# Performance work log

Measured on AMD Instinct MI355X. Metric: run time of the kernel, lower is better.

Reference implementation:

```python
import jax, jax.numpy as jnp
import numpy as np

N_NODES = 100000


def _gcn_edges(edge_index, num_nodes):
    # Add self-loops and compute symmetric GCN normalization per edge.
    src = jnp.concatenate([edge_index[0], jnp.arange(num_nodes, dtype=edge_index.dtype)])
    dst = jnp.concatenate([edge_index[1], jnp.arange(num_nodes, dtype=edge_index.dtype)])
    deg = jnp.zeros((num_nodes,), jnp.float32).at[dst].add(1.0)
    dinv = jnp.where(deg > 0, jax.lax.rsqrt(deg), 0.0)
    norm = dinv[src] * dinv[dst]  # [E+N]
    return src, dst, norm


def _gcn_conv(x, W, b, src, dst, norm, num_nodes):
    h = x @ W                         # [N, d_out] transform first (d_out <= d_in)
    msg = h[src] * norm[:, None]      # [E, d_out] gather + scale
    agg = jax.ops.segment_sum(msg, dst, num_segments=num_nodes)
    return agg + b


def setup_inputs() -> dict:
    key = jax.random.key(0)
    k = jax.random.split(key, 8)
    n, e, d_in, d_out = N_NODES, 1600000, 128, 64
    hid = 2 * d_out
    s = lambda fan: 1.0 / np.sqrt(fan)
    return {
        "x": jax.random.normal(k[0], (n, d_in), jnp.float32),
        "edge_index": jax.random.randint(k[1], (2, e), 0, n, jnp.int64),
        "W1": jax.random.normal(k[2], (d_in, hid), jnp.float32) * s(d_in),
        "b1": jnp.zeros((hid,), jnp.float32),
        "Wmu": jax.random.normal(k[3], (hid, d_out), jnp.float32) * s(hid),
        "bmu": jnp.zeros((d_out,), jnp.float32),
        "Wls": jax.random.normal(k[4], (hid, d_out), jnp.float32) * s(hid),
        "bls": jnp.zeros((d_out,), jnp.float32),
    }


def reference(x, edge_index, W1, b1, Wmu, bmu, Wls, bls):
    n = x.shape[0]
    src, dst, norm = _gcn_edges(edge_index, n)
    h = jax.nn.relu(_gcn_conv(x, W1, b1, src, dst, norm, n))
    mu = _gcn_conv(h, Wmu, bmu, src, dst, norm, n)
    logstd = _gcn_conv(h, Wls, bls, src, dst, norm, n)
    return mu, logstd
```

## Files before the change

kernel.cpp:

```cpp
#include <hip/hip_runtime.h>

#define DIN 128
#define HID 128
#define DOUT 64
#define NCHUNK 784
#define BSH 9
#define NB1MAX 256
#define BSLACK 1540

typedef unsigned short ushort_t;
typedef unsigned int uint_t;
typedef __attribute__((ext_vector_type(4))) short s4v;
typedef __attribute__((ext_vector_type(4))) float f4v;

#if defined(__has_builtin)
#if __has_builtin(__builtin_amdgcn_mfma_f32_16x16x16bf16_1k)
#define MFMA16(a, b, c) __builtin_amdgcn_mfma_f32_16x16x16bf16_1k(a, b, c, 0, 0, 0)
#endif
#endif
#ifndef MFMA16
static __device__ inline f4v mfma16_asm(s4v a, s4v b, f4v c) {
  asm volatile("v_mfma_f32_16x16x16_bf16 %0, %1, %2, %0" : "+v"(c) : "v"(a), "v"(b));
  return c;
}
#define MFMA16(a, b, c) mfma16_asm(a, b, c)
#endif

static inline int ceil_div(int a, int b) { return (a + b - 1) / b; }

__device__ inline ushort_t f2bf(float f) {
  uint_t u = __float_as_uint(f);
  u += 0x7fff + ((u >> 16) & 1);
  return (ushort_t)(u >> 16);
}
__device__ inline uint_t pack2bf(float a, float b) {
  return (uint_t)f2bf(a) | ((uint_t)f2bf(b) << 16);
}
__device__ inline float2 bf2x2(uint_t u) {
  return make_float2(__uint_as_float(u << 16), __uint_as_float(u & 0xffff0000u));
}

__device__ inline int blk_scan_incl(int v, int* ws, int nw) {
  int t = threadIdx.x, lane = t & 63, w = t >> 6;
#pragma unroll
  for (int d = 1; d < 64; d <<= 1) {
    int u = __shfl_up(v, d, 64);
    if (lane >= d) v += u;
  }
  if (lane == 63) ws[w] = v;
  __syncthreads();
  if (w == 0) {
    int s = (lane < nw) ? ws[lane] : 0;
    for (int d = 1; d < nw; d <<= 1) {
      int u = __shfl_up(s, d, 64);
      if (lane >= d) s += u;
    }
    if (lane < nw) ws[lane] = s;
  }
  __syncthreads();
  if (w > 0) v += ws[w - 1];
  return v;
}


__global__ __launch_bounds__(512) void k_setup(const int* __restrict__ dst, int E, int CH,
                                               int nb1, int* __restrict__ counts,
                                               const float* __restrict__ x,
                                               const float* __restrict__ W1,
                                               const float* __restrict__ Wmu,
                                               const float* __restrict__ Wls,
                                               ushort_t* __restrict__ Wt2,
                                               ushort_t* __restrict__ xWb,
                                               ushort_t* __restrict__ h,
                                               float* __restrict__ dinv, int N, int G1) {
  __shared__ ushort_t Ws[128][132];
  __shared__ uint_t cnt[NB1MAX];
  int b = blockIdx.x, t = threadIdx.x;
  if (b < G1) {
#pragma unroll
    for (int it = 0; it < 16; it++) {
      int k = it * 8 + ((t >> 7) << 1);
      int j = t & 127;
      float a = W1[k * 128 + j];
      float bb = W1[(k + 1) * 128 + j];
      *(uint_t*)&Ws[j][k] = pack2bf(a, bb);
    }
    __syncthreads();
    int w = t >> 6, lane = t & 63;
    int rl = lane & 15, g = lane >> 4;
    int row = b * 128 + w * 16 + rl;
    bool valid = row < N;
    const float* Ar = x + (size_t)row * DIN + 4 * g;
    s4v af[8];
#pragma unroll
    for (int kk = 0; kk < 8; kk++) {
      float4 v = make_float4(0.f, 0.f, 0.f, 0.f);
      if (valid) v = *(const float4*)(Ar + kk * 16);
      s4v a;
      a[0] = (short)f2bf(v.x);
      a[1] = (short)f2bf(v.y);
      a[2] = (short)f2bf(v.z);
      a[3] = (short)f2bf(v.w);
      af[kk] = a;
    }
    f4v acc[8];
#pragma unroll
    for (int ct = 0; ct < 8; ct++) acc[ct] = (f4v)0.f;
#pragma unroll
    for (int kk = 0; kk < 8; kk++) {
      int ko = kk * 16 + 4 * g;
#pragma unroll
      for (int ct = 0; ct < 8; ct++) {
        s4v bb = *(s4v*)&Ws[ct * 16 + rl][ko];
        acc[ct] = MFMA16(af[kk], bb, acc[ct]);
      }
    }
    int gr0 = b * 128 + w * 16 + 4 * g;
#pragma unroll
    for (int i = 0; i < 4; i++) {
      int gr = gr0 + i;
      if (gr < N) {
#pragma unroll
        for (int ct = 0; ct < 8; ct++)
          xWb[(size_t)gr * HID + ct * 16 + rl] = f2bf(acc[ct][i]);
      }
    }
  } else if (b < G1 + NCHUNK) {
    int c = b - G1;
    for (int i = t; i < nb1; i += 512) cnt[i] = 0;
    __syncthreads();
    int e0 = c * CH, e1 = min(E, e0 + CH);
    for (int i = e0 + t; i < e1; i += 512) atomicAdd(&cnt[((uint_t)dst[i]) >> BSH], 1u);
    __syncthreads();
    for (int i = t; i < nb1; i += 512) counts[c * nb1 + i] = (int)cnt[i];
  } else if (b < G1 + NCHUNK + 32) {
    int idx = (b - G1 - NCHUNK) * 512 + t;
    int j = idx >> 7, k = idx & 127;
    Wt2[j * 128 + k] = f2bf(j < 64 ? Wmu[k * 64 + j] : Wls[k * 64 + (j - 64)]);
  } else {
    if (t < 64) ((uint_t*)(xWb + (size_t)N * HID))[t] = 0;
    else if (t < 128) ((uint_t*)(h + (size_t)N * HID))[t - 64] = 0;
    else if (t == 128) dinv[N] = 0.f;
  }
}

__global__ __launch_bounds__(256) void k_bscan(const int* __restrict__ counts, int nb1,
                                               int* __restrict__ chunk_off,
                                               int* __restrict__ btot) {
  __shared__ int ws[8];
  __shared__ int shc;
  int b = blockIdx.x, t = threadIdx.x;
  int carry = 0;
#pragma unroll
  for (int r = 0; r < NCHUNK / 256 + 1; r++) {
    int idx = r * 256 + t;
    int v = (idx < NCHUNK) ? counts[idx * nb1 + b] : 0;
    int incl = blk_scan_incl(v, ws, 4) + carry;
    if (idx < NCHUNK) chunk_off[idx * nb1 + b] = incl - v;
    if (t == 255) shc = incl;
    __syncthreads();
    carry = shc;
  }
  if (t == 0) btot[b] = carry;
}

__global__ __launch_bounds__(256) void k_bscatter(const int* __restrict__ src,
                                                  const int* __restrict__ dst, int E, int CH,
                                                  int nb1, const int* __restrict__ btot,
                                                  const int* __restrict__ chunk_off,
                                                  uint_t* __restrict__ tmp) {
  __shared__ int ws[8];
  __shared__ uint_t cur[NB1MAX];
  int t = threadIdx.x, c = blockIdx.x;
  {
    int v = (t < nb1) ? btot[t] : 0;
    int incl = blk_scan_incl(v, ws, 4);
    if (t < nb1) cur[t] = (uint_t)(incl - v + chunk_off[c * nb1 + t]);
  }
  __syncthreads();
  int e0 = c * CH, e1 = min(E, e0 + CH);
  for (int i = e0 + t; i < e1; i += 256) {
    uint_t d = (uint_t)dst[i];
    uint_t s = (uint_t)src[i];
    uint_t p = atomicAdd(&cur[d >> BSH], 1u);
    tmp[p] = ((d & ((1u << BSH) - 1)) << 17) | s;
  }
}

__global__ __launch_bounds__(512) void k_bfinal(const uint_t* __restrict__ tmp,
                                                const int* __restrict__ btot, int N, int nb1,
                                                uint_t* __restrict__ csr,
                                                int* __restrict__ row_ptr,
                                                int* __restrict__ row_end,
                                                float* __restrict__ dinv) {
  __shared__ int ws[8];
  __shared__ int sseg0, sseg1;
  __shared__ uint_t cnt[1 << BSH];
  __shared__ uint_t ppfx[1 << BSH];
  __shared__ uint_t cur[1 << BSH];
  int b = blockIdx.x, t = threadIdx.x;
  {
    int v = (t < nb1) ? btot[t] : 0;
    int incl = blk_scan_incl(v, ws, 8);
    if (t == b) {
      sseg0 = incl - v;
      sseg1 = incl;
    }
  }
  for (int i = t; i < (1 << BSH); i += 512) cnt[i] = 0;
  __syncthreads();
  int seg0 = sseg0, seg1 = sseg1;
  int pb = ((seg0 + 3) & ~3) + BSLACK * b;
  for (int i = seg0 + t; i < seg1; i += 512) atomicAdd(&cnt[tmp[i] >> 17], 1u);
  __syncthreads();
  if (t < 64) {
    uint_t pc[8];
    uint_t s = 0;
#pragma unroll
    for (int k = 0; k < 8; k++) {
      pc[k] = (cnt[t * 8 + k] + 3u) & ~3u;
      s += pc[k];
    }
    int incl = (int)s;
#pragma unroll
    for (int d = 1; d < 64; d <<= 1) {
      int u = __shfl_up(incl, d, 64);
      if (t >= d) incl += u;
    }
    uint_t excl = (uint_t)incl - s;
#pragma unroll
    for (int k = 0; k < 8; k++) {
      ppfx[t * 8 + k] = excl;
      excl += pc[k];
    }
  }
  __syncthreads();
  int nd0 = b << BSH;
  for (int i = t; i < (1 << BSH); i += 512) {
    cur[i] = ppfx[i];
    int g = nd0 + i;
    if (g < N) {
      row_ptr[g] = pb + (int)ppfx[i];
      row_end[g] = pb + (int)(ppfx[i] + ((cnt[i] + 3u) & ~3u));
      dinv[g] = rsqrtf((float)cnt[i] + 1.0f);
    }
  }
  __syncthreads();
  for (int i = seg0 + t; i < seg1; i += 512) {
    uint_t v = tmp[i];
    uint_t pos = atomicAdd(&cur[v >> 17], 1u);
    csr[pb + (int)pos] = v & 0x1FFFFu;
  }
  __syncthreads();
  for (int i = t; i < (1 << BSH); i += 512) {
    uint_t e0 = cur[i];
    uint_t e1 = ppfx[i] + ((cnt[i] + 3u) & ~3u);
    for (uint_t k = e0; k < e1; k++) csr[pb + (int)k] = (uint_t)N;
  }
}


__global__ __launch_bounds__(256) void k_agg(const ushort_t* __restrict__ H,
                                             const int* __restrict__ row_ptr,
                                             const int* __restrict__ row_end,
                                             const uint_t* __restrict__ csr,
                                             const float* __restrict__ dinv,
                                             const float* __restrict__ bias,
                                             ushort_t* __restrict__ out, int n) {
  int node = (blockIdx.x * blockDim.x + threadIdx.x) >> 6;
  int lane = threadIdx.x & 63;
  if (node >= n) return;
  const char* Hb = (const char*)H;
  const char* Db = (const char*)dinv;
  uint_t loff = (uint_t)lane << 2;
  float dn = dinv[node];
  int j = row_ptr[node], end = row_end[node];
  float2 hs = bf2x2(*(const uint_t*)(Hb + ((size_t)(((uint_t)node << 8) | loff))));
  float ax = dn * hs.x, ay = dn * hs.y;
  if (j < end) {
    uint4 c = *(const uint4*)(csr + j);
    while (true) {
      int jn = j + 4;
      bool more = jn < end;
      uint4 cn;
      if (more) cn = *(const uint4*)(csr + jn);
      float w0 = *(const float*)(Db + (size_t)(c.x << 2));
      float w1 = *(const float*)(Db + (size_t)(c.y << 2));
      float w2 = *(const float*)(Db + (size_t)(c.z << 2));
      float w3 = *(const float*)(Db + (size_t)(c.w << 2));
      uint_t v0 = *(const uint_t*)(Hb + (size_t)((c.x << 8) | loff));
      uint_t v1 = *(const uint_t*)(Hb + (size_t)((c.y << 8) | loff));
      uint_t v2 = *(const uint_t*)(Hb + (size_t)((c.z << 8) | loff));
      uint_t v3 = *(const uint_t*)(Hb + (size_t)((c.w << 8) | loff));
      float2 f0 = bf2x2(v0), f1 = bf2x2(v1), f2 = bf2x2(v2), f3 = bf2x2(v3);
      ax += w0 * f0.x; ay += w0 * f0.y;
      ax += w1 * f1.x; ay += w1 * f1.y;
      ax += w2 * f2.x; ay += w2 * f2.y;
      ax += w3 * f3.x; ay += w3 * f3.y;
      if (!more) break;
      c = cn;
      j = jn;
    }
  }
  ax = fmaxf(dn * ax + bias[2 * lane], 0.f) * dn;
  ay = fmaxf(dn * ay + bias[2 * lane + 1], 0.f) * dn;
  ((uint_t*)out)[(size_t)node * 64 + lane] = pack2bf(ax, ay);
}


__global__ __launch_bounds__(1024) void k_agg2g(const ushort_t* __restrict__ H,
                                                const int* __restrict__ row_ptr,
                                                const int* __restrict__ row_end,
                                                const uint_t* __restrict__ csr,
                                                const float* __restrict__ dinv,
                                                const ushort_t* __restrict__ Wt2,
                                                const float* __restrict__ bmu,
                                                const float* __restrict__ bls,
                                                float* __restrict__ out, int n) {
  __shared__ ushort_t rows[16][132];
  int t = threadIdx.x, w = t >> 6, lane = t & 63;
  int node = blockIdx.x * 16 + w;
  float ax = 0.f, ay = 0.f;
  if (node < n) {
    const char* Hb = (const char*)H;
    uint_t loff = (uint_t)lane << 2;
    float dn = dinv[node];
    int j = row_ptr[node], end = row_end[node];
    float2 hs = bf2x2(*(const uint_t*)(Hb + ((size_t)(((uint_t)node << 8) | loff))));
    ax = hs.x;
    ay = hs.y;
    if (j < end) {
      uint4 c = *(const uint4*)(csr + j);
      while (true) {
        int jn = j + 4;
        bool more = jn < end;
        uint4 cn;
        if (more) cn = *(const uint4*)(csr + jn);
        uint_t v0 = *(const uint_t*)(Hb + (size_t)((c.x << 8) | loff));
        uint_t v1 = *(const uint_t*)(Hb + (size_t)((c.y << 8) | loff));
        uint_t v2 = *(const uint_t*)(Hb + (size_t)((c.z << 8) | loff));
        uint_t v3 = *(const uint_t*)(Hb + (size_t)((c.w << 8) | loff));
        float2 f0 = bf2x2(v0), f1 = bf2x2(v1), f2 = bf2x2(v2), f3 = bf2x2(v3);
        ax += f0.x + f1.x;
        ay += f0.y + f1.y;
        ax += f2.x + f3.x;
        ay += f2.y + f3.y;
        if (!more) break;
        c = cn;
        j = jn;
      }
    }
    ax *= dn;
    ay *= dn;
  }
  *(uint_t*)&rows[w][2 * lane] = pack2bf(ax, ay);
  __syncthreads();
  if (w < 8) {
    int ct = w, rl = lane & 15, g = lane >> 4;
    f4v acc = (f4v)0.f;
#pragma unroll
    for (int kk = 0; kk < 8; kk++) {
      s4v a = *(s4v*)&rows[rl][kk * 16 + 4 * g];
      s4v b = *(const s4v*)(Wt2 + (size_t)(ct * 16 + rl) * 128 + kk * 16 + 4 * g);
      acc = MFMA16(a, b, acc);
    }
    int col = ct * 16 + rl;
    float bv = (col < 64) ? bmu[col] : bls[col - 64];
    size_t obase = (col < 64) ? 0 : (size_t)n * DOUT;
    int cc = col & 63;
#pragma unroll
    for (int i = 0; i < 4; i++) {
      int nd = blockIdx.x * 16 + 4 * g + i;
      if (nd < n) out[obase + (size_t)nd * DOUT + cc] = acc[i] + bv;
    }
  }
}


extern "C" void kernel_launch(void* const* d_in, const int* in_sizes, int n_in,
                              void* d_out, int out_size, void* d_ws, size_t ws_size,
                              hipStream_t stream) {
  const float* x   = (const float*)d_in[0];
  const int*   ei  = (const int*)d_in[1];
  const float* W1  = (const float*)d_in[2];
  const float* b1  = (const float*)d_in[3];
  const float* Wmu = (const float*)d_in[4];
  const float* bmu = (const float*)d_in[5];
  const float* Wls = (const float*)d_in[6];
  const float* bls = (const float*)d_in[7];
  float* out = (float*)d_out;

  const int N = in_sizes[0] / DIN;
  const int E = in_sizes[1] / 2;
  const int* esrc = ei;
  const int* edst = ei + E;
  const int nb1 = ceil_div(N, 1 << BSH);
  const int CH = ceil_div(E, NCHUNK);
  const int G1 = ceil_div(N, 128);

  char* ws = (char*)d_ws;
  size_t off = 0;
  auto alloc = [&](size_t bytes) -> void* {
    void* p = ws + off;
    off = (off + bytes + 255) & ~(size_t)255;
    return p;
  };
  ushort_t* xWb   = (ushort_t*)alloc((size_t)(N + 1) * HID * sizeof(ushort_t));
  ushort_t* h     = (ushort_t*)alloc((size_t)(N + 1) * HID * sizeof(ushort_t));
  uint_t* csr     = (uint_t*)alloc(((size_t)E + (size_t)(BSLACK + 8) * nb1 + 16) * 4);
  uint_t* tmp     = (uint_t*)alloc((size_t)E * 4);
  int* counts     = (int*)alloc((size_t)NCHUNK * nb1 * 4);
  int* chunk_off  = (int*)alloc((size_t)NCHUNK * nb1 * 4);
  int* btot       = (int*)alloc((size_t)nb1 * 4);
  int* row_ptr    = (int*)alloc((size_t)N * 4);
  int* row_end    = (int*)alloc((size_t)N * 4);
  float* dinv     = (float*)alloc((size_t)(N + 1) * 4);
  ushort_t* wt2b  = (ushort_t*)alloc((size_t)HID * HID * 2);
  (void)ws_size; (void)n_in; (void)out_size;

  k_setup<<<G1 + NCHUNK + 33, 512, 0, stream>>>(edst, E, CH, nb1, counts, x, W1, Wmu, Wls,
                                                wt2b, xWb, h, dinv, N, G1);
  k_bscan<<<nb1, 256, 0, stream>>>(counts, nb1, chunk_off, btot);
  k_bscatter<<<NCHUNK, 256, 0, stream>>>(esrc, edst, E, CH, nb1, btot, chunk_off, tmp);
  k_bfinal<<<nb1, 512, 0, stream>>>(tmp, btot, N, nb1, csr, row_ptr, row_end, dinv);

  k_agg<<<ceil_div(N, 4), 256, 0, stream>>>(xWb, row_ptr, row_end, csr, dinv, b1, h, N);

  k_agg2g<<<ceil_div(N, 16), 1024, 0, stream>>>(h, row_ptr, row_end, csr, dinv, wt2b, bmu, bls,
                                                out, N);
}
```

Baseline: 249.4 us.

## Split fused layer-2 aggregate+GEMM into separate aggregation and MFMA GEMM kernels

The fused layer-2 kernel, which aggregated 16 nodes per 1024-thread block and then ran a small MFMA GEMM on 8 of its 16 waves, is split in two. One 256-thread kernel does the neighbour aggregation and writes bf16 rows into the xWb buffer. A separate GEMM kernel stages the weight matrix in LDS and computes 64 rows by 128 columns per block with MFMA. The aim is to remove the block-wide barrier and the idle waves during the GEMM, which limited latency hiding in the gather. The cost is an extra kernel launch and a round trip through global memory for the intermediate.

```diff
diff --git a/kernel.cpp b/kernel.cpp
--- a/kernel.cpp
+++ b/kernel.cpp
@@ -260,13 +260,13 @@
 }
 
 
-__global__ __launch_bounds__(256) void k_agg(const ushort_t* __restrict__ H,
-                                             const int* __restrict__ row_ptr,
-                                             const int* __restrict__ row_end,
-                                             const uint_t* __restrict__ csr,
-                                             const float* __restrict__ dinv,
-                                             const float* __restrict__ bias,
-                                             ushort_t* __restrict__ out, int n) {
+__global__ __launch_bounds__(256) void k_agg1(const ushort_t* __restrict__ H,
+                                              const int* __restrict__ row_ptr,
+                                              const int* __restrict__ row_end,
+                                              const uint_t* __restrict__ csr,
+                                              const float* __restrict__ dinv,
+                                              const float* __restrict__ bias,
+                                              ushort_t* __restrict__ out, int n) {
   int node = (blockIdx.x * blockDim.x + threadIdx.x) >> 6;
   int lane = threadIdx.x & 63;
   if (node >= n) return;
@@ -308,70 +308,106 @@
 }
 
 
-__global__ __launch_bounds__(1024) void k_agg2g(const ushort_t* __restrict__ H,
-                                                const int* __restrict__ row_ptr,
-                                                const int* __restrict__ row_end,
-                                                const uint_t* __restrict__ csr,
-                                                const float* __restrict__ dinv,
-                                                const ushort_t* __restrict__ Wt2,
-                                                const float* __restrict__ bmu,
-                                                const float* __restrict__ bls,
-                                                float* __restrict__ out, int n) {
-  __shared__ ushort_t rows[16][132];
-  int t = threadIdx.x, w = t >> 6, lane = t & 63;
-  int node = blockIdx.x * 16 + w;
-  float ax = 0.f, ay = 0.f;
-  if (node < n) {
-    const char* Hb = (const char*)H;
-    uint_t loff = (uint_t)lane << 2;
-    float dn = dinv[node];
-    int j = row_ptr[node], end = row_end[node];
-    float2 hs = bf2x2(*(const uint_t*)(Hb + ((size_t)(((uint_t)node << 8) | loff))));
-    ax = hs.x;
-    ay = hs.y;
-    if (j < end) {
-      uint4 c = *(const uint4*)(csr + j);
-      while (true) {
-        int jn = j + 4;
-        bool more = jn < end;
-        uint4 cn;
-        if (more) cn = *(const uint4*)(csr + jn);
-        uint_t v0 = *(const uint_t*)(Hb + (size_t)((c.x << 8) | loff));
-        uint_t v1 = *(const uint_t*)(Hb + (size_t)((c.y << 8) | loff));
-        uint_t v2 = *(const uint_t*)(Hb + (size_t)((c.z << 8) | loff));
-        uint_t v3 = *(const uint_t*)(Hb + (size_t)((c.w << 8) | loff));
-        float2 f0 = bf2x2(v0), f1 = bf2x2(v1), f2 = bf2x2(v2), f3 = bf2x2(v3);
-        ax += f0.x + f1.x;
-        ay += f0.y + f1.y;
-        ax += f2.x + f3.x;
-        ay += f2.y + f3.y;
-        if (!more) break;
-        c = cn;
-        j = jn;
-      }
-    }
-    ax *= dn;
-    ay *= dn;
-  }
-  *(uint_t*)&rows[w][2 * lane] = pack2bf(ax, ay);
-  __syncthreads();
-  if (w < 8) {
-    int ct = w, rl = lane & 15, g = lane >> 4;
-    f4v acc = (f4v)0.f;
-#pragma unroll
-    for (int kk = 0; kk < 8; kk++) {
-      s4v a = *(s4v*)&rows[rl][kk * 16 + 4 * g];
-      s4v b = *(const s4v*)(Wt2 + (size_t)(ct * 16 + rl) * 128 + kk * 16 + 4 * g);
-      acc = MFMA16(a, b, acc);
-    }
+__global__ __launch_bounds__(256) void k_agg2(const ushort_t* __restrict__ H,
+                                              const int* __restrict__ row_ptr,
+                                              const int* __restrict__ row_end,
+                                              const uint_t* __restrict__ csr,
+                                              const float* __restrict__ dinv,
+                                              ushort_t* __restrict__ out, int n) {
+  int node = (blockIdx.x * blockDim.x + threadIdx.x) >> 6;
+  int lane = threadIdx.x & 63;
+  if (node >= n) return;
+  const char* Hb = (const char*)H;
+  uint_t loff = (uint_t)lane << 2;
+  float dn = dinv[node];
+  int j = row_ptr[node], end = row_end[node];
+  float2 hs = bf2x2(*(const uint_t*)(Hb + ((size_t)(((uint_t)node << 8) | loff))));
+  float ax = hs.x, ay = hs.y;
+  if (j < end) {
+    uint4 c = *(const uint4*)(csr + j);
+    while (true) {
+      int jn = j + 4;
+      bool more = jn < end;
+      uint4 cn;
+      if (more) cn = *(const uint4*)(csr + jn);
+      uint_t v0 = *(const uint_t*)(Hb + (size_t)((c.x << 8) | loff));
+      uint_t v1 = *(const uint_t*)(Hb + (size_t)((c.y << 8) | loff));
+      uint_t v2 = *(const uint_t*)(Hb + (size_t)((c.z << 8) | loff));
+      uint_t v3 = *(const uint_t*)(Hb + (size_t)((c.w << 8) | loff));
+      float2 f0 = bf2x2(v0), f1 = bf2x2(v1), f2 = bf2x2(v2), f3 = bf2x2(v3);
+      ax += f0.x + f1.x;
+      ay += f0.y + f1.y;
+      ax += f2.x + f3.x;
+      ay += f2.y + f3.y;
+      if (!more) break;
+      c = cn;
+      j = jn;
+    }
+  }
+  ax *= dn;
+  ay *= dn;
+  ((uint_t*)out)[(size_t)node * 64 + lane] = pack2bf(ax, ay);
+}
+
+
+__global__ __launch_bounds__(256) void k_gemm2(const ushort_t* __restrict__ A,
+                                               const ushort_t* __restrict__ Wt,
+                                               const float* __restrict__ bmu,
+                                               const float* __restrict__ bls,
+                                               float* __restrict__ out, int n) {
+  __shared__ ushort_t Ws[128][132];
+  int t = threadIdx.x;
+#pragma unroll
+  for (int i = 0; i < 16; i++) {
+    int f = t + 256 * i;
+    int rowj = f >> 5, seg = f & 31;
+    *(uint2*)&Ws[rowj][seg * 4] = *(const uint2*)(Wt + rowj * 128 + seg * 4);
+  }
+  __syncthreads();
+  int w = t >> 6, lane = t & 63;
+  int rl = lane & 15, g = lane >> 4;
+  int row = blockIdx.x * 64 + w * 16 + rl;
+  bool valid = row < n;
+  const ushort_t* Ar = A + (size_t)row * HID + 4 * g;
+  s4v af[8];
+#pragma unroll
+  for (int kk = 0; kk < 8; kk++) {
+    s4v a = (s4v)0;
+    if (valid) a = *(const s4v*)(Ar + kk * 16);
+    af[kk] = a;
+  }
+  f4v acc[8];
+#pragma unroll
+  for (int ct = 0; ct < 8; ct++) acc[ct] = (f4v)0.f;
+#pragma unroll
+  for (int kk = 0; kk < 8; kk++) {
+    int ko = kk * 16 + 4 * g;
+#pragma unroll
+    for (int ct = 0; ct < 8; ct++) {
+      s4v b = *(s4v*)&Ws[ct * 16 + rl][ko];
+      acc[ct] = MFMA16(af[kk], b, acc[ct]);
+    }
+  }
+  int gr0 = blockIdx.x * 64 + w * 16 + 4 * g;
+#pragma unroll
+  for (int ct = 0; ct < 8; ct++) {
     int col = ct * 16 + rl;
-    float bv = (col < 64) ? bmu[col] : bls[col - 64];
-    size_t obase = (col < 64) ? 0 : (size_t)n * DOUT;
-    int cc = col & 63;
+    float bv;
+    size_t obase;
+    int cc;
+    if (ct < 4) {
+      bv = bmu[col];
+      obase = 0;
+      cc = col;
+    } else {
+      bv = bls[col - 64];
+      obase = (size_t)n * DOUT;
+      cc = col - 64;
+    }
 #pragma unroll
     for (int i = 0; i < 4; i++) {
-      int nd = blockIdx.x * 16 + 4 * g + i;
-      if (nd < n) out[obase + (size_t)nd * DOUT + cc] = acc[i] + bv;
+      int gr = gr0 + i;
+      if (gr < n) out[obase + (size_t)gr * DOUT + cc] = acc[ct][i] + bv;
     }
   }
 }
@@ -424,8 +460,8 @@
   k_bscatter<<<NCHUNK, 256, 0, stream>>>(esrc, edst, E, CH, nb1, btot, chunk_off, tmp);
   k_bfinal<<<nb1, 512, 0, stream>>>(tmp, btot, N, nb1, csr, row_ptr, row_end, dinv);
 
-  k_agg<<<ceil_div(N, 4), 256, 0, stream>>>(xWb, row_ptr, row_end, csr, dinv, b1, h, N);
-
-  k_agg2g<<<ceil_div(N, 16), 1024, 0, stream>>>(h, row_ptr, row_end, csr, dinv, wt2b, bmu, bls,
-                                                out, N);
-}
+  k_agg1<<<ceil_div(N, 4), 256, 0, stream>>>(xWb, row_ptr, row_end, csr, dinv, b1, h, N);
+
+  k_agg2<<<ceil_div(N, 4), 256, 0, stream>>>(h, row_ptr, row_end, csr, dinv, xWb, N);
+  k_gemm2<<<ceil_div(N, 64), 256, 0, stream>>>(xWb, wt2b, bmu, bls, out, N);
+}
```

After: 214.0 us. 1.17x faster.
